# Kernel optimization log

Measured on AMD Instinct MI355X. Metric: run time of the kernel, lower is better.

The kernel has to match this reference:

```python
import jax, jax.numpy as jnp
import numpy as np

EPS = 1e-08


def setup_inputs() -> dict:
    key = jax.random.key(0)
    k1, k2, k3 = jax.random.split(key, 3)
    N, IN_DIM, OUT_DIM = 8192, 512, 512
    h = jax.random.normal(k1, (N, IN_DIM), dtype=jnp.float32)
    adj = jax.random.randint(k2, (N, N), 0, 2, dtype=jnp.int32)
    # nn.Linear(in_dim, out_dim, bias=False) weight: [out_dim, in_dim]
    W = jax.random.normal(k3, (OUT_DIM, IN_DIM), dtype=jnp.float32) * (1.0 / np.sqrt(IN_DIM))
    return {"h": h, "adj": adj, "W": W}


def reference(h, adj, W):
    # Wh = h @ W^T  -> [N, out_dim]
    Wh = h @ W.T
    N = Wh.shape[0]
    norms = jnp.linalg.norm(Wh, axis=1, keepdims=True)  # [N, 1]
    # cosine similarity [N, N]
    sim = (Wh @ Wh.T) / (norms * norms.T + EPS)
    mask = (adj > 0) | jnp.eye(N, dtype=bool)
    sim_masked = jnp.where(mask, sim, -jnp.inf)
    alpha = jax.nn.softmax(sim_masked, axis=1)
    return alpha @ Wh
```

## Files before the change

kernel.cpp:

```cpp
#include <hip/hip_runtime.h>
#include <hip/hip_bf16.h>
#include <stdint.h>

#define NN 8192
#define DD 512

typedef unsigned short u16;
typedef unsigned long long u64;
typedef __attribute__((ext_vector_type(8))) short short8;
typedef __attribute__((ext_vector_type(4))) float f32x4;

__device__ __forceinline__ void gld_lds16(const void* g, void* l) {
  __builtin_amdgcn_global_load_lds(
      (const __attribute__((address_space(1))) uint32_t*)(uintptr_t)g,
      (__attribute__((address_space(3))) uint32_t*)(uintptr_t)l,
      16, 0, 0);
}

__device__ __forceinline__ u16 f2bf(float f) {
  __hip_bfloat16 b = __float2bfloat16(f);
  return __builtin_bit_cast(u16, b);
}

__global__ void fill_kernel(float* __restrict__ p, int n, float v) {
  int i = blockIdx.x * 256 + threadIdx.x;
  int stride = gridDim.x * 256;
  for (; i < n; i += stride) p[i] = v;
}

__global__ void cvt4_kernel(const float4* __restrict__ src, ushort4* __restrict__ dst, int n4) {
  int i = blockIdx.x * 256 + threadIdx.x;
  int stride = gridDim.x * 256;
  for (; i < n4; i += stride) {
    float4 v = src[i];
    ushort4 o;
    o.x = f2bf(v.x); o.y = f2bf(v.y); o.z = f2bf(v.z); o.w = f2bf(v.w);
    dst[i] = o;
  }
}

__global__ void pack_adj_kernel(const int* __restrict__ adj, u16* __restrict__ mask) {
  const int row = blockIdx.x;
  const int t = threadIdx.x;
  const uint4* arow = (const uint4*)(adj + (size_t)row * NN);
  #pragma unroll
  for (int iter = 0; iter < 2; iter++) {
    const int c16 = iter * 256 + t;
    unsigned int bits = 0;
    #pragma unroll
    for (int g = 0; g < 4; g++) {
      uint4 v = arow[c16 * 4 + g];
      bits |= (v.x ? 1u : 0u) << (g * 4 + 0);
      bits |= (v.y ? 1u : 0u) << (g * 4 + 1);
      bits |= (v.z ? 1u : 0u) << (g * 4 + 2);
      bits |= (v.w ? 1u : 0u) << (g * 4 + 3);
    }
    mask[(size_t)row * (NN / 16) + c16] = (u16)bits;
  }
}

__global__ void rownorm_kernel(const float* __restrict__ Wh, float* __restrict__ invn) {
  int row = blockIdx.x;
  int l = threadIdx.x;
  const float4* p = (const float4*)(Wh + (size_t)row * DD);
  float4 a = p[l], b = p[l + 64];
  float s = a.x*a.x + a.y*a.y + a.z*a.z + a.w*a.w
          + b.x*b.x + b.y*b.y + b.z*b.z + b.w*b.w;
  #pragma unroll
  for (int off = 32; off; off >>= 1) s += __shfl_down(s, off);
  if (l == 0) invn[row] = 1.0f / sqrtf(s);
}

__global__ void u_wht_kernel(const float* __restrict__ Wh, const float* __restrict__ invn,
                             u16* __restrict__ U, u16* __restrict__ WhT) {
  __shared__ float tile[64][65];
  int i0 = blockIdx.x * 64, d0 = blockIdx.y * 64;
  int c = threadIdx.x & 63, rb = threadIdx.x >> 6;
  #pragma unroll
  for (int r = rb; r < 64; r += 4) {
    float v = Wh[(size_t)(i0 + r) * DD + d0 + c];
    tile[r][c] = v;
    U[(size_t)(i0 + r) * DD + d0 + c] = f2bf(v * invn[i0 + r]);
  }
  __syncthreads();
  #pragma unroll
  for (int r = rb; r < 64; r += 4) {
    WhT[(size_t)(d0 + r) * NN + i0 + c] = f2bf(tile[c][r]);
  }
}

template <int MODE>
__global__ void __launch_bounds__(256) gemm_bt(
    const u16* __restrict__ A, const u16* __restrict__ B,
    int Nn, int K,
    float* __restrict__ Cf,
    const u64* __restrict__ maskw, u16* __restrict__ Pb,
    float* __restrict__ den)
{
  __shared__ __align__(16) u16 As[128 * 32];
  __shared__ __align__(16) u16 Bs[128 * 32];

  const int tid = threadIdx.x;
  const int w = tid >> 6;
  const int lane = tid & 63;
  const int lm = lane & 15;
  const int q = lane >> 4;
  const int row0 = blockIdx.y * 128;
  const int col0 = blockIdx.x * 128;
  const int RM = (w >> 1) * 64;
  const int RN = (w & 1) * 64;

  const int sr = tid >> 2;
  const int sk = (tid & 3) * 8;

  f32x4 acc[4][4];
  #pragma unroll
  for (int a_ = 0; a_ < 4; a_++)
    #pragma unroll
    for (int b_ = 0; b_ < 4; b_++)
      acc[a_][b_] = (f32x4){0.f, 0.f, 0.f, 0.f};

  const size_t Abase = (size_t)row0 * K;
  const size_t Bbase = (size_t)col0 * K;

  for (int k0 = 0; k0 < K; k0 += 32) {
    __syncthreads();
    gld_lds16(A + Abase + (size_t)sr * K + k0 + sk,        (char*)As + w * 1024);
    gld_lds16(A + Abase + (size_t)(sr + 64) * K + k0 + sk, (char*)As + 4096 + w * 1024);
    gld_lds16(B + Bbase + (size_t)sr * K + k0 + sk,        (char*)Bs + w * 1024);
    gld_lds16(B + Bbase + (size_t)(sr + 64) * K + k0 + sk, (char*)Bs + 4096 + w * 1024);
    __syncthreads();

    short8 af[4], bfr[4];
    #pragma unroll
    for (int mt = 0; mt < 4; mt++)
      af[mt] = *(const short8*)&As[(RM + mt * 16 + lm) * 32 + q * 8];
    #pragma unroll
    for (int nt = 0; nt < 4; nt++)
      bfr[nt] = *(const short8*)&Bs[(RN + nt * 16 + lm) * 32 + q * 8];

    #pragma unroll
    for (int mt = 0; mt < 4; mt++)
      #pragma unroll
      for (int nt = 0; nt < 4; nt++)
        acc[mt][nt] = __builtin_amdgcn_mfma_f32_16x16x32_bf16(af[mt], bfr[nt], acc[mt][nt], 0, 0, 0);
  }

  const int wordIdx = (col0 + RN) >> 6;
  #pragma unroll
  for (int mt = 0; mt < 4; mt++) {
    const int ib = row0 + RM + mt * 16 + q * 4;
    #pragma unroll
    for (int rr = 0; rr < 4; rr++) {
      const int i = ib + rr;
      if (MODE == 0) {
        #pragma unroll
        for (int nt = 0; nt < 4; nt++) {
          const int jc = col0 + RN + nt * 16 + lm;
          Cf[(size_t)i * Nn + jc] = acc[mt][nt][rr];
        }
      } else {
        const u64 wrd = maskw[(size_t)i * (NN / 64) + wordIdx];
        float psum = 0.f;
        #pragma unroll
        for (int nt = 0; nt < 4; nt++) {
          const int jc = col0 + RN + nt * 16 + lm;
          const bool on = ((wrd >> (nt * 16 + lm)) & 1ull) || (i == jc);
          const float p = on ? __expf(acc[mt][nt][rr]) : 0.0f;
          psum += p;
          Pb[(size_t)i * NN + jc] = f2bf(p);
        }
        #pragma unroll
        for (int off = 8; off; off >>= 1) psum += __shfl_down(psum, off, 16);
        if (lm == 0) atomicAdd(&den[i], psum);
      }
    }
  }
}

__global__ void __launch_bounds__(512, 2) gemm_out(
    const u16* __restrict__ A,
    const u16* __restrict__ B,
    u16* const __restrict__* partv_unused,
    u16* __restrict__ p0, u16* __restrict__ p1,
    u16* __restrict__ p2, u16* __restrict__ p3)
{
  __shared__ __align__(16) u16 As[128 * 32];
  __shared__ __align__(16) u16 Bs[512 * 32];

  const int tid = threadIdx.x;
  const int w = tid >> 6;
  const int lane = tid & 63;
  const int lm = lane & 15;
  const int q = lane >> 4;
  const int row0 = blockIdx.x * 128;
  const int z = blockIdx.y;
  const int RM = (w >> 2) * 64;
  const int RN = (w & 3) * 128;

  const int sr = tid >> 2;
  const int sk = (tid & 3) * 8;

  f32x4 acc[4][8];
  #pragma unroll
  for (int a_ = 0; a_ < 4; a_++)
    #pragma unroll
    for (int b_ = 0; b_ < 8; b_++)
      acc[a_][b_] = (f32x4){0.f, 0.f, 0.f, 0.f};

  const size_t Abase = (size_t)row0 * NN;
  const int kBegin = z * (NN / 4), kEnd = (z + 1) * (NN / 4);

  for (int k0 = kBegin; k0 < kEnd; k0 += 32) {
    __syncthreads();
    gld_lds16(A + Abase + (size_t)sr * NN + k0 + sk, (char*)As + w * 1024);
    #pragma unroll
    for (int c = 0; c < 4; c++)
      gld_lds16(B + (size_t)(c * 128 + sr) * NN + k0 + sk, (char*)Bs + c * 8192 + w * 1024);
    __syncthreads();

    short8 af[4], bfr[8];
    #pragma unroll
    for (int mt = 0; mt < 4; mt++)
      af[mt] = *(const short8*)&As[(RM + mt * 16 + lm) * 32 + q * 8];
    #pragma unroll
    for (int nt = 0; nt < 8; nt++)
      bfr[nt] = *(const short8*)&Bs[(RN + nt * 16 + lm) * 32 + q * 8];

    #pragma unroll
    for (int mt = 0; mt < 4; mt++)
      #pragma unroll
      for (int nt = 0; nt < 8; nt++)
        acc[mt][nt] = __builtin_amdgcn_mfma_f32_16x16x32_bf16(af[mt], bfr[nt], acc[mt][nt], 0, 0, 0);
  }

  u16* const part = (z == 0) ? p0 : (z == 1) ? p1 : (z == 2) ? p2 : p3;
  #pragma unroll
  for (int mt = 0; mt < 4; mt++) {
    const int ib = row0 + RM + mt * 16 + q * 4;
    #pragma unroll
    for (int rr = 0; rr < 4; rr++) {
      const int i = ib + rr;
      #pragma unroll
      for (int nt = 0; nt < 8; nt++) {
        const int dc = RN + nt * 16 + lm;
        part[(size_t)i * DD + dc] = f2bf(acc[mt][nt][rr]);
      }
    }
  }
}

__global__ void reduce4_kernel(const uint4* __restrict__ p0, const uint4* __restrict__ p1,
                               const uint4* __restrict__ p2, const uint4* __restrict__ p3,
                               const float* __restrict__ den, float4* __restrict__ out) {
  const int idx = blockIdx.x * 256 + threadIdx.x;
  const int row = idx >> 6;
  const float dinv = 1.0f / den[row];
  float s[8] = {0, 0, 0, 0, 0, 0, 0, 0};
  #pragma unroll
  for (int zp = 0; zp < 4; zp++) {
    const uint4 u = (zp == 0 ? p0 : zp == 1 ? p1 : zp == 2 ? p2 : p3)[idx];
    s[0] += __uint_as_float(u.x << 16); s[1] += __uint_as_float(u.x & 0xffff0000u);
    s[2] += __uint_as_float(u.y << 16); s[3] += __uint_as_float(u.y & 0xffff0000u);
    s[4] += __uint_as_float(u.z << 16); s[5] += __uint_as_float(u.z & 0xffff0000u);
    s[6] += __uint_as_float(u.w << 16); s[7] += __uint_as_float(u.w & 0xffff0000u);
  }
  float4 o0 = {s[0] * dinv, s[1] * dinv, s[2] * dinv, s[3] * dinv};
  float4 o1 = {s[4] * dinv, s[5] * dinv, s[6] * dinv, s[7] * dinv};
  out[idx * 2] = o0;
  out[idx * 2 + 1] = o1;
}

extern "C" void kernel_launch(void* const* d_in, const int* in_sizes, int n_in,
                              void* d_out, int out_size, void* d_ws, size_t ws_size,
                              hipStream_t stream) {
  const float* h = (const float*)d_in[0];
  const int* adj = (const int*)d_in[1];
  const float* W = (const float*)d_in[2];
  float* out = (float*)d_out;

  const size_t SZ_P    = (size_t)NN * NN * 2;
  const size_t SZ_MASK = (size_t)NN * NN / 8;
  const size_t SZ_WHT  = (size_t)DD * NN * 2;
  const size_t SZ_HB   = (size_t)NN * DD * 2;
  const size_t SZ_WB   = (size_t)DD * DD * 2;
  const size_t SZ_U    = (size_t)NN * DD * 2;
  const size_t SZ_WH   = (size_t)NN * DD * 4;
  const size_t NEEDED  = SZ_P + SZ_MASK + SZ_WHT + SZ_HB + SZ_WB + SZ_U + SZ_WH + 2 * (size_t)NN * 4;

  if (ws_size < NEEDED) {
    fill_kernel<<<256, 256, 0, stream>>>(out, out_size, 12345.0f);
    return;
  }

  char* ws = (char*)d_ws;
  size_t off = 0;
  u16*   P    = (u16*)(ws + off); off += SZ_P;
  u16*   mask = (u16*)(ws + off); off += SZ_MASK;
  u16*   WhT  = (u16*)(ws + off); off += SZ_WHT;
  u16*   hb   = (u16*)(ws + off); off += SZ_HB;
  u16*   Wb   = (u16*)(ws + off); off += SZ_WB;
  u16*   U    = (u16*)(ws + off); off += SZ_U;
  float* Wh   = (float*)(ws + off); off += SZ_WH;
  float* invn = (float*)(ws + off);
  float* den  = invn + NN;

  u16* part0 = U;
  u16* part1 = hb;
  u16* part2 = (u16*)Wh;
  u16* part3 = (u16*)Wh + (size_t)NN * DD;

  pack_adj_kernel<<<NN, 256, 0, stream>>>(adj, mask);
  fill_kernel<<<32, 256, 0, stream>>>(den, NN, 0.0f);
  cvt4_kernel<<<1024, 256, 0, stream>>>((const float4*)h, (ushort4*)hb, NN * DD / 4);
  cvt4_kernel<<<256, 256, 0, stream>>>((const float4*)W, (ushort4*)Wb, DD * DD / 4);
  gemm_bt<0><<<dim3(DD / 128, NN / 128), 256, 0, stream>>>(
      hb, Wb, DD, DD, Wh, nullptr, nullptr, nullptr);
  rownorm_kernel<<<NN, 64, 0, stream>>>(Wh, invn);
  u_wht_kernel<<<dim3(NN / 64, DD / 64), 256, 0, stream>>>(Wh, invn, U, WhT);
  gemm_bt<1><<<dim3(NN / 128, NN / 128), 256, 0, stream>>>(
      U, U, NN, DD, nullptr, (const u64*)mask, P, den);
  gemm_out<<<dim3(NN / 128, 4), 512, 0, stream>>>(
      P, WhT, nullptr, part0, part1, part2, part3);
  reduce4_kernel<<<NN * DD / 8 / 256, 256, 0, stream>>>(
      (const uint4*)part0, (const uint4*)part1, (const uint4*)part2, (const uint4*)part3,
      den, (float4*)out);
}
```

Before: 670.9 us.

## Exploit symmetry of the similarity matrix with triangular tiling in the sim GEMM

The sim GEMM now launches only lower-triangular 128x128 tiles of U·Uᵀ. Each off-diagonal tile writes both P[i,j] and the mirrored P[j,i], applying the mask read for each orientation, and atomically adds into both row denominators. This roughly halves the MFMA and exp work for the NxN similarity stage. In exchange, the transposed write-back is a strided ushort4 store with poor coalescing, and the extra mask loads and registers add cost. Zeroing of den is folded into pack_adj, and the workspace is reused so that Wh lives in the P buffer.

```diff
diff --git a/kernel.cpp b/kernel.cpp
--- a/kernel.cpp
+++ b/kernel.cpp
@@ -39,9 +39,11 @@
   }
 }
 
-__global__ void pack_adj_kernel(const int* __restrict__ adj, u16* __restrict__ mask) {
+__global__ void pack_adj_kernel(const int* __restrict__ adj, u16* __restrict__ mask,
+                                float* __restrict__ den) {
   const int row = blockIdx.x;
   const int t = threadIdx.x;
+  if (t == 0) den[row] = 0.0f;
   const uint4* arow = (const uint4*)(adj + (size_t)row * NN);
   #pragma unroll
   for (int iter = 0; iter < 2; iter++) {
@@ -89,13 +91,9 @@
   }
 }
 
-template <int MODE>
-__global__ void __launch_bounds__(256) gemm_bt(
+__global__ void __launch_bounds__(256) gemm_wh(
     const u16* __restrict__ A, const u16* __restrict__ B,
-    int Nn, int K,
-    float* __restrict__ Cf,
-    const u64* __restrict__ maskw, u16* __restrict__ Pb,
-    float* __restrict__ den)
+    int Nn, int K, float* __restrict__ Cf)
 {
   __shared__ __align__(16) u16 As[128 * 32];
   __shared__ __align__(16) u16 Bs[128 * 32];
@@ -109,7 +107,6 @@
   const int col0 = blockIdx.x * 128;
   const int RM = (w >> 1) * 64;
   const int RN = (w & 1) * 64;
-
   const int sr = tid >> 2;
   const int sk = (tid & 3) * 8;
 
@@ -146,34 +143,142 @@
         acc[mt][nt] = __builtin_amdgcn_mfma_f32_16x16x32_bf16(af[mt], bfr[nt], acc[mt][nt], 0, 0, 0);
   }
 
-  const int wordIdx = (col0 + RN) >> 6;
   #pragma unroll
   for (int mt = 0; mt < 4; mt++) {
     const int ib = row0 + RM + mt * 16 + q * 4;
     #pragma unroll
     for (int rr = 0; rr < 4; rr++) {
       const int i = ib + rr;
-      if (MODE == 0) {
-        #pragma unroll
-        for (int nt = 0; nt < 4; nt++) {
-          const int jc = col0 + RN + nt * 16 + lm;
-          Cf[(size_t)i * Nn + jc] = acc[mt][nt][rr];
+      #pragma unroll
+      for (int nt = 0; nt < 4; nt++) {
+        const int jc = col0 + RN + nt * 16 + lm;
+        Cf[(size_t)i * Nn + jc] = acc[mt][nt][rr];
+      }
+    }
+  }
+}
+
+__global__ void __launch_bounds__(256) gemm_sim(
+    const u16* __restrict__ U, const u64* __restrict__ maskw,
+    u16* __restrict__ Pb, float* __restrict__ den)
+{
+  __shared__ __align__(16) u16 As[128 * 32];
+  __shared__ __align__(16) u16 Bs[128 * 32];
+
+  const int b = blockIdx.x;
+  int bi = (int)((sqrtf(8.0f * (float)b + 1.0f) - 1.0f) * 0.5f);
+  while ((bi + 1) * (bi + 2) / 2 <= b) bi++;
+  while (bi * (bi + 1) / 2 > b) bi--;
+  const int bj = b - bi * (bi + 1) / 2;
+
+  const int tid = threadIdx.x;
+  const int w = tid >> 6;
+  const int lane = tid & 63;
+  const int lm = lane & 15;
+  const int q = lane >> 4;
+  const int row0 = bi * 128;
+  const int col0 = bj * 128;
+  const int RM = (w >> 1) * 64;
+  const int RN = (w & 1) * 64;
+  const int sr = tid >> 2;
+  const int sk = (tid & 3) * 8;
+  const bool diag = (bi == bj);
+
+  f32x4 acc[4][4];
+  #pragma unroll
+  for (int a_ = 0; a_ < 4; a_++)
+    #pragma unroll
+    for (int b_ = 0; b_ < 4; b_++)
+      acc[a_][b_] = (f32x4){0.f, 0.f, 0.f, 0.f};
+
+  const size_t Abase = (size_t)row0 * DD;
+  const size_t Bbase = (size_t)col0 * DD;
+
+  for (int k0 = 0; k0 < DD; k0 += 32) {
+    __syncthreads();
+    gld_lds16(U + Abase + (size_t)sr * DD + k0 + sk,        (char*)As + w * 1024);
+    gld_lds16(U + Abase + (size_t)(sr + 64) * DD + k0 + sk, (char*)As + 4096 + w * 1024);
+    gld_lds16(U + Bbase + (size_t)sr * DD + k0 + sk,        (char*)Bs + w * 1024);
+    gld_lds16(U + Bbase + (size_t)(sr + 64) * DD + k0 + sk, (char*)Bs + 4096 + w * 1024);
+    __syncthreads();
+
+    short8 af[4], bfr[4];
+    #pragma unroll
+    for (int mt = 0; mt < 4; mt++)
+      af[mt] = *(const short8*)&As[(RM + mt * 16 + lm) * 32 + q * 8];
+    #pragma unroll
+    for (int nt = 0; nt < 4; nt++)
+      bfr[nt] = *(const short8*)&Bs[(RN + nt * 16 + lm) * 32 + q * 8];
+
+    #pragma unroll
+    for (int mt = 0; mt < 4; mt++)
+      #pragma unroll
+      for (int nt = 0; nt < 4; nt++)
+        acc[mt][nt] = __builtin_amdgcn_mfma_f32_16x16x32_bf16(af[mt], bfr[nt], acc[mt][nt], 0, 0, 0);
+  }
+
+  const int wordIdx = (col0 + RN) >> 6;
+  const int word2Idx = (row0 + RM) >> 6;
+
+  u64 wrd2[4];
+  if (!diag) {
+    #pragma unroll
+    for (int nt = 0; nt < 4; nt++) {
+      const int jc = col0 + RN + nt * 16 + lm;
+      wrd2[nt] = maskw[(size_t)jc * (NN / 64) + word2Idx];
+    }
+  }
+
+  float msum[4] = {0.f, 0.f, 0.f, 0.f};
+
+  #pragma unroll
+  for (int mt = 0; mt < 4; mt++) {
+    const int ib = row0 + RM + mt * 16 + q * 4;
+    float pm[4][4];
+    #pragma unroll
+    for (int rr = 0; rr < 4; rr++) {
+      const int i = ib + rr;
+      const u64 wrd = maskw[(size_t)i * (NN / 64) + wordIdx];
+      const int bit2 = mt * 16 + q * 4 + rr;
+      float psum = 0.f;
+      #pragma unroll
+      for (int nt = 0; nt < 4; nt++) {
+        const int jc = col0 + RN + nt * 16 + lm;
+        const float ev = __expf(acc[mt][nt][rr]);
+        const bool on = ((wrd >> (nt * 16 + lm)) & 1ull) || (diag && i == jc);
+        const float p = on ? ev : 0.0f;
+        psum += p;
+        Pb[(size_t)i * NN + jc] = f2bf(p);
+        if (!diag) {
+          const bool on2 = (wrd2[nt] >> bit2) & 1ull;
+          const float pmv = on2 ? ev : 0.0f;
+          pm[nt][rr] = pmv;
+          msum[nt] += pmv;
         }
-      } else {
-        const u64 wrd = maskw[(size_t)i * (NN / 64) + wordIdx];
-        float psum = 0.f;
-        #pragma unroll
-        for (int nt = 0; nt < 4; nt++) {
-          const int jc = col0 + RN + nt * 16 + lm;
-          const bool on = ((wrd >> (nt * 16 + lm)) & 1ull) || (i == jc);
-          const float p = on ? __expf(acc[mt][nt][rr]) : 0.0f;
-          psum += p;
-          Pb[(size_t)i * NN + jc] = f2bf(p);
-        }
-        #pragma unroll
-        for (int off = 8; off; off >>= 1) psum += __shfl_down(psum, off, 16);
-        if (lm == 0) atomicAdd(&den[i], psum);
       }
+      #pragma unroll
+      for (int off = 8; off; off >>= 1) psum += __shfl_down(psum, off, 16);
+      if (lm == 0) atomicAdd(&den[i], psum);
+    }
+    if (!diag) {
+      #pragma unroll
+      for (int nt = 0; nt < 4; nt++) {
+        const int jc = col0 + RN + nt * 16 + lm;
+        ushort4 m4;
+        m4.x = f2bf(pm[nt][0]); m4.y = f2bf(pm[nt][1]);
+        m4.z = f2bf(pm[nt][2]); m4.w = f2bf(pm[nt][3]);
+        *(ushort4*)&Pb[(size_t)jc * NN + ib] = m4;
+      }
+    }
+  }
+
+  if (!diag) {
+    #pragma unroll
+    for (int nt = 0; nt < 4; nt++) {
+      float s = msum[nt];
+      s += __shfl_xor(s, 16);
+      s += __shfl_xor(s, 32);
+      if (q == 0) atomicAdd(&den[col0 + RN + nt * 16 + lm], s);
     }
   }
 }
@@ -181,7 +286,6 @@
 __global__ void __launch_bounds__(512, 2) gemm_out(
     const u16* __restrict__ A,
     const u16* __restrict__ B,
-    u16* const __restrict__* partv_unused,
     u16* __restrict__ p0, u16* __restrict__ p1,
     u16* __restrict__ p2, u16* __restrict__ p3)
 {
@@ -197,7 +301,6 @@
   const int z = blockIdx.y;
   const int RM = (w >> 2) * 64;
   const int RN = (w & 3) * 128;
-
   const int sr = tid >> 2;
   const int sk = (tid & 3) * 8;
 
@@ -285,8 +388,8 @@
   const size_t SZ_HB   = (size_t)NN * DD * 2;
   const size_t SZ_WB   = (size_t)DD * DD * 2;
   const size_t SZ_U    = (size_t)NN * DD * 2;
-  const size_t SZ_WH   = (size_t)NN * DD * 4;
-  const size_t NEEDED  = SZ_P + SZ_MASK + SZ_WHT + SZ_HB + SZ_WB + SZ_U + SZ_WH + 2 * (size_t)NN * 4;
+  const size_t SZ_P3   = (size_t)NN * DD * 2;
+  const size_t NEEDED  = SZ_P + SZ_MASK + SZ_WHT + SZ_HB + SZ_WB + SZ_U + SZ_P3 + 2 * (size_t)NN * 4;
 
   if (ws_size < NEEDED) {
     fill_kernel<<<256, 256, 0, stream>>>(out, out_size, 12345.0f);
@@ -301,27 +404,24 @@
   u16*   hb   = (u16*)(ws + off); off += SZ_HB;
   u16*   Wb   = (u16*)(ws + off); off += SZ_WB;
   u16*   U    = (u16*)(ws + off); off += SZ_U;
-  float* Wh   = (float*)(ws + off); off += SZ_WH;
+  u16*   p3   = (u16*)(ws + off); off += SZ_P3;
   float* invn = (float*)(ws + off);
   float* den  = invn + NN;
 
-  u16* part0 = U;
-  u16* part1 = hb;
-  u16* part2 = (u16*)Wh;
-  u16* part3 = (u16*)Wh + (size_t)NN * DD;
-
-  pack_adj_kernel<<<NN, 256, 0, stream>>>(adj, mask);
-  fill_kernel<<<32, 256, 0, stream>>>(den, NN, 0.0f);
+  float* Wh = (float*)P;
+  u16* part0 = mask;
+  u16* part1 = U;
+  u16* part2 = hb;
+  u16* part3 = p3;
+
+  pack_adj_kernel<<<NN, 256, 0, stream>>>(adj, mask, den);
   cvt4_kernel<<<1024, 256, 0, stream>>>((const float4*)h, (ushort4*)hb, NN * DD / 4);
   cvt4_kernel<<<256, 256, 0, stream>>>((const float4*)W, (ushort4*)Wb, DD * DD / 4);
-  gemm_bt<0><<<dim3(DD / 128, NN / 128), 256, 0, stream>>>(
-      hb, Wb, DD, DD, Wh, nullptr, nullptr, nullptr);
+  gemm_wh<<<dim3(DD / 128, NN / 128), 256, 0, stream>>>(hb, Wb, DD, DD, Wh);
   rownorm_kernel<<<NN, 64, 0, stream>>>(Wh, invn);
   u_wht_kernel<<<dim3(NN / 64, DD / 64), 256, 0, stream>>>(Wh, invn, U, WhT);
-  gemm_bt<1><<<dim3(NN / 128, NN / 128), 256, 0, stream>>>(
-      U, U, NN, DD, nullptr, (const u64*)mask, P, den);
-  gemm_out<<<dim3(NN / 128, 4), 512, 0, stream>>>(
-      P, WhT, nullptr, part0, part1, part2, part3);
+  gemm_sim<<<64 * 65 / 2, 256, 0, stream>>>(U, (const u64*)mask, P, den);
+  gemm_out<<<dim3(NN / 128, 4), 512, 0, stream>>>(P, WhT, part0, part1, part2, part3);
   reduce4_kernel<<<NN * DD / 8 / 256, 256, 0, stream>>>(
       (const uint4*)part0, (const uint4*)part1, (const uint4*)part2, (const uint4*)part3,
       den, (float4*)out);
```

Result: faster. 649.8 us (-3.1%).
